# Performance work log

Hardware: AMD Instinct MI355X
Metric: run time of the kernel (lower is better)

## Reference

```python
import jax, jax.numpy as jnp
import numpy as np

B, H, W, C = 3072, 64, 64, 3  # kernel_size=64 forces H=W=64; reshape forces B % 3 == 0


def setup_inputs() -> dict:
    key = jax.random.key(0)
    k0, k1, k2, k3, k4 = jax.random.split(key, 5)
    inputs = jax.random.normal(k0, (B, H, W, C), dtype=jnp.float32)
    # Conv2D(filters=3, kernel_size=64) params, HWIO layout
    w1 = jax.random.normal(k1, (64, 64, 3, 3), dtype=jnp.float32) * 0.02
    b1 = jax.random.normal(k2, (3,), dtype=jnp.float32) * 0.02
    w2 = jax.random.normal(k3, (64, 64, 3, 3), dtype=jnp.float32) * 0.02
    b2 = jax.random.normal(k4, (3,), dtype=jnp.float32) * 0.02
    return {"inputs": inputs, "w1": w1, "b1": b1, "w2": w2, "b2": b2}


def _hilbert_axis1(x):
    # FFT-based Hilbert transform along axis=1 (analytic-signal filter), N even
    N = x.shape[1]
    h = np.zeros(N, dtype=np.float32)
    h[0] = h[N // 2] = 1.0
    h[1:N // 2] = 2.0
    hf = jnp.asarray(h)[None, :, None, None]
    Xf = jnp.fft.fft(x, axis=1)
    return jnp.imag(jnp.fft.ifft(Xf * hf, axis=1)).astype(x.dtype)


def reference(inputs, w1, b1, w2, b2):
    maps_x = inputs[..., :3]                                  # [B,64,64,3]
    b_, h_, w_, c_ = maps_x.shape
    # kernel covers the whole 64x64 image -> 1x1 conv output == full contraction
    v1 = jnp.einsum('bhwc,hwcf->bf', maps_x, w1) + b1          # [B,3]
    v2 = jnp.einsum('bhwc,hwcf->bf', maps_x, w2) + b2          # [B,3]
    V = jnp.stack([v1, v2], axis=-1)                           # [B,3,2]
    V = V / (1e-6 + jnp.sum(jnp.abs(V), axis=1, keepdims=True))
    mx_t = maps_x.reshape(b_, h_ * w_, c_).transpose(0, 2, 1)  # [B,3,HW]
    # Gram matrix and closed-form 2x2 inverse (math of tf.linalg.inv on [B,2,2])
    G = jnp.einsum('bci,bcj->bij', V, V)                       # [B,2,2]
    a = G[:, 0, 0]; bb = G[:, 0, 1]; c = G[:, 1, 0]; d = G[:, 1, 1]
    det = a * d - bb * c
    Ginv = jnp.stack([jnp.stack([d, -bb], -1),
                      jnp.stack([-c, a], -1)], 1) / det[:, None, None]  # [B,2,2]
    Vt_x = jnp.einsum('bck,bcn->bkn', V, mx_t)                 # [B,2,HW]
    rec_t = jnp.einsum('bck,bkn->bcn', V, Ginv @ Vt_x)         # [B,3,HW]
    # lstsq(V, rec_t) via normal equations (tf fast lstsq): z = Ginv V^T rec_t
    z = Ginv @ jnp.einsum('bck,bcn->bkn', V, rec_t)            # [B,2,HW]
    rec = z.transpose(0, 2, 1).reshape(-1, h_, w_, c_)         # [2B/3,64,64,3]
    rec_h = _hilbert_axis1(rec)
    return jnp.concatenate([rec, rec_h], axis=-1)              # [2B/3,64,64,6]
```

## Files before the change

kernel.cpp:

```cpp
#include <hip/hip_runtime.h>
#include <math.h>

#define B_TOT 3072
#define PIX   12288

__global__ __launch_bounds__(256) void compute_M_kernel(
    const float* __restrict__ x, const float* __restrict__ w1,
    const float* __restrict__ b1, const float* __restrict__ w2,
    const float* __restrict__ b2, float* __restrict__ Mout) {
  const int b = blockIdx.x;
  const float4* xb4 = (const float4*)(x + (size_t)b * PIX);
  const float4* w14 = (const float4*)w1;
  const float4* w24 = (const float4*)w2;
  float s[6] = {0, 0, 0, 0, 0, 0};
  for (int i4 = threadIdx.x; i4 < PIX / 4; i4 += 256) {
    float4 xv = xb4[i4];
    float4 a0 = w14[i4 * 3 + 0], a1 = w14[i4 * 3 + 1], a2 = w14[i4 * 3 + 2];
    float4 c0 = w24[i4 * 3 + 0], c1 = w24[i4 * 3 + 1], c2 = w24[i4 * 3 + 2];
    s[0] += xv.x * a0.x + xv.y * a0.w + xv.z * a1.z + xv.w * a2.y;
    s[1] += xv.x * a0.y + xv.y * a1.x + xv.z * a1.w + xv.w * a2.z;
    s[2] += xv.x * a0.z + xv.y * a1.y + xv.z * a2.x + xv.w * a2.w;
    s[3] += xv.x * c0.x + xv.y * c0.w + xv.z * c1.z + xv.w * c2.y;
    s[4] += xv.x * c0.y + xv.y * c1.x + xv.z * c1.w + xv.w * c2.z;
    s[5] += xv.x * c0.z + xv.y * c1.y + xv.z * c2.x + xv.w * c2.w;
  }
  double sd[6];
  #pragma unroll
  for (int j = 0; j < 6; ++j) {
    sd[j] = (double)s[j];
    #pragma unroll
    for (int off = 32; off > 0; off >>= 1)
      sd[j] += __shfl_down(sd[j], off, 64);
  }
  __shared__ double wred[4][6];
  const int wave = threadIdx.x >> 6, lane = threadIdx.x & 63;
  if (lane == 0) {
    #pragma unroll
    for (int j = 0; j < 6; ++j) wred[wave][j] = sd[j];
  }
  __syncthreads();
  if (threadIdx.x == 0) {
    double v[3][2];
    for (int c = 0; c < 3; ++c) {
      v[c][0] = wred[0][c] + wred[1][c] + wred[2][c] + wred[3][c] + (double)b1[c];
      v[c][1] = wred[0][3 + c] + wred[1][3 + c] + wred[2][3 + c] + wred[3][3 + c] + (double)b2[c];
    }
    for (int k = 0; k < 2; ++k) {
      double l1 = 1e-6 + fabs(v[0][k]) + fabs(v[1][k]) + fabs(v[2][k]);
      for (int c = 0; c < 3; ++c) v[c][k] /= l1;
    }
    double G00 = 0, G01 = 0, G11 = 0;
    for (int c = 0; c < 3; ++c) {
      G00 += v[c][0] * v[c][0];
      G01 += v[c][0] * v[c][1];
      G11 += v[c][1] * v[c][1];
    }
    double det = G00 * G11 - G01 * G01;
    double i00 = G11 / det, i01 = -G01 / det, i11 = G00 / det;
    float* Mo = Mout + (size_t)b * 6;
    for (int c = 0; c < 3; ++c) {
      Mo[0 * 3 + c] = (float)(i00 * v[c][0] + i01 * v[c][1]);
      Mo[1 * 3 + c] = (float)(i01 * v[c][0] + i11 * v[c][1]);
    }
  }
}

__global__ __launch_bounds__(192) void z_hilbert_kernel(
    const float* __restrict__ x, const float* __restrict__ M,
    float* __restrict__ out) {
  const int b2 = blockIdx.x;
  __shared__ float rec[PIX];
  __shared__ float Ms[12];
  const size_t zbase = (size_t)b2 * PIX;
  const int b_lo = (int)(zbase >> 13);
  if (threadIdx.x < 12) {
    int bb = b_lo + (int)(threadIdx.x / 6);
    float mv = 0.f;
    if (bb < B_TOT) mv = M[(size_t)bb * 6 + (threadIdx.x % 6)];
    Ms[threadIdx.x] = mv;
  }
  __syncthreads();
  float* outb = out + (size_t)b2 * 24576;

  for (int j = threadIdx.x; j < PIX / 2; j += 192) {
    int ml = j << 1;
    size_t m = zbase + (size_t)ml;
    int b = (int)(m >> 13);
    int n = (int)((m & 8191) >> 1);
    int wb = (b - b_lo) * 6;
    const float* xp = x + (size_t)b * PIX + n * 3;
    float x0 = xp[0], x1 = xp[1], x2 = xp[2];
    float r0 = Ms[wb + 0] * x0 + Ms[wb + 1] * x1 + Ms[wb + 2] * x2;
    float r1 = Ms[wb + 3] * x0 + Ms[wb + 4] * x1 + Ms[wb + 5] * x2;
    float2 rr; rr.x = r0; rr.y = r1;
    ((float2*)rec)[j] = rr;
  }
  __syncthreads();

  {
    const int col = threadIdx.x;
    const int w = col / 3, c = col % 3;
    float gc[16];
    #pragma unroll
    for (int jj = 0; jj < 16; ++jj) {
      float ang = 3.14159265358979323846f * (float)(2 * jj + 1) / 64.0f;
      gc[jj] = 0.03125f * cosf(ang) / sinf(ang);
    }
    float v[64];
    #pragma unroll
    for (int h = 0; h < 64; ++h) v[h] = rec[h * 192 + col];
    float* oc = outb + w * 6 + c;
    #pragma unroll
    for (int h = 0; h < 64; ++h) {
      float acc = 0.f;
      #pragma unroll
      for (int jj = 0; jj < 16; ++jj) {
        int d = 2 * jj + 1;
        acc += gc[jj] * (v[(h - d) & 63] - v[(h + d) & 63]);
      }
      oc[h * 384 + 0] = v[h];
      oc[h * 384 + 3] = acc;
    }
  }
}

extern "C" void kernel_launch(void* const* d_in, const int* in_sizes, int n_in,
                              void* d_out, int out_size, void* d_ws, size_t ws_size,
                              hipStream_t stream) {
  const float* x  = (const float*)d_in[0];
  const float* w1 = (const float*)d_in[1];
  const float* b1 = (const float*)d_in[2];
  const float* w2 = (const float*)d_in[3];
  const float* b2 = (const float*)d_in[4];
  float* out = (float*)d_out;
  float* M = (float*)d_ws;

  compute_M_kernel<<<B_TOT, 256, 0, stream>>>(x, w1, b1, w2, b2, M);
  z_hilbert_kernel<<<2048, 192, 0, stream>>>(x, M, out);
}
```

Measured before the change: 397.2 us.

## Vectorize loads and stores, float shuffle reductions, and nontemporal output writes

In the first kernel the contraction loop is unrolled and the warp reduction uses float shuffles instead of double. The second kernel now runs 256 threads: the rec build reads the input as float4 and writes float4 to shared memory, and the Hilbert stage uses 48 lanes per wave. Those lanes exchange neighbour values with shuffles so each thread writes a contiguous float2 to the output with nontemporal stores. The aim is to cut the number of memory transactions and the cost of the double-precision shuffles, at the price of a quarter of the lanes idling during the Hilbert stage and slightly less precise partial sums.

New measurement: 373.9 us. 5.9% less time.

```diff
diff --git a/kernel.cpp b/kernel.cpp
--- a/kernel.cpp
+++ b/kernel.cpp
@@ -3,6 +3,8 @@
 
 #define B_TOT 3072
 #define PIX   12288
+
+typedef float v2f __attribute__((ext_vector_type(2)));
 
 __global__ __launch_bounds__(256) void compute_M_kernel(
     const float* __restrict__ x, const float* __restrict__ w1,
@@ -13,6 +15,7 @@
   const float4* w14 = (const float4*)w1;
   const float4* w24 = (const float4*)w2;
   float s[6] = {0, 0, 0, 0, 0, 0};
+  #pragma unroll 4
   for (int i4 = threadIdx.x; i4 < PIX / 4; i4 += 256) {
     float4 xv = xb4[i4];
     float4 a0 = w14[i4 * 3 + 0], a1 = w14[i4 * 3 + 1], a2 = w14[i4 * 3 + 2];
@@ -24,26 +27,26 @@
     s[4] += xv.x * c0.y + xv.y * c1.x + xv.z * c1.w + xv.w * c2.z;
     s[5] += xv.x * c0.z + xv.y * c1.y + xv.z * c2.x + xv.w * c2.w;
   }
-  double sd[6];
   #pragma unroll
   for (int j = 0; j < 6; ++j) {
-    sd[j] = (double)s[j];
     #pragma unroll
     for (int off = 32; off > 0; off >>= 1)
-      sd[j] += __shfl_down(sd[j], off, 64);
+      s[j] += __shfl_down(s[j], off, 64);
   }
-  __shared__ double wred[4][6];
+  __shared__ float wred[4][6];
   const int wave = threadIdx.x >> 6, lane = threadIdx.x & 63;
   if (lane == 0) {
     #pragma unroll
-    for (int j = 0; j < 6; ++j) wred[wave][j] = sd[j];
+    for (int j = 0; j < 6; ++j) wred[wave][j] = s[j];
   }
   __syncthreads();
   if (threadIdx.x == 0) {
     double v[3][2];
     for (int c = 0; c < 3; ++c) {
-      v[c][0] = wred[0][c] + wred[1][c] + wred[2][c] + wred[3][c] + (double)b1[c];
-      v[c][1] = wred[0][3 + c] + wred[1][3 + c] + wred[2][3 + c] + wred[3][3 + c] + (double)b2[c];
+      v[c][0] = (double)wred[0][c] + (double)wred[1][c] + (double)wred[2][c] +
+                (double)wred[3][c] + (double)b1[c];
+      v[c][1] = (double)wred[0][3 + c] + (double)wred[1][3 + c] +
+                (double)wred[2][3 + c] + (double)wred[3][3 + c] + (double)b2[c];
     }
     for (int k = 0; k < 2; ++k) {
       double l1 = 1e-6 + fabs(v[0][k]) + fabs(v[1][k]) + fabs(v[2][k]);
@@ -65,11 +68,11 @@
   }
 }
 
-__global__ __launch_bounds__(192) void z_hilbert_kernel(
+__global__ __launch_bounds__(256) void z_hilbert_kernel(
     const float* __restrict__ x, const float* __restrict__ M,
     float* __restrict__ out) {
   const int b2 = blockIdx.x;
-  __shared__ float rec[PIX];
+  __shared__ __align__(16) float rec[PIX];
   __shared__ float Ms[12];
   const size_t zbase = (size_t)b2 * PIX;
   const int b_lo = (int)(zbase >> 13);
@@ -82,24 +85,36 @@
   __syncthreads();
   float* outb = out + (size_t)b2 * 24576;
 
-  for (int j = threadIdx.x; j < PIX / 2; j += 192) {
-    int ml = j << 1;
+  for (int g = threadIdx.x; g < PIX / 8; g += 256) {
+    int ml = g << 3;
     size_t m = zbase + (size_t)ml;
     int b = (int)(m >> 13);
-    int n = (int)((m & 8191) >> 1);
+    int n0 = (int)((m & 8191) >> 1);
     int wb = (b - b_lo) * 6;
-    const float* xp = x + (size_t)b * PIX + n * 3;
-    float x0 = xp[0], x1 = xp[1], x2 = xp[2];
-    float r0 = Ms[wb + 0] * x0 + Ms[wb + 1] * x1 + Ms[wb + 2] * x2;
-    float r1 = Ms[wb + 3] * x0 + Ms[wb + 4] * x1 + Ms[wb + 5] * x2;
-    float2 rr; rr.x = r0; rr.y = r1;
-    ((float2*)rec)[j] = rr;
+    float m00 = Ms[wb + 0], m01 = Ms[wb + 1], m02 = Ms[wb + 2];
+    float m10 = Ms[wb + 3], m11 = Ms[wb + 4], m12 = Ms[wb + 5];
+    const float4* xp = (const float4*)(x + (size_t)b * PIX + (size_t)n0 * 3);
+    float4 p0 = xp[0], p1 = xp[1], p2 = xp[2];
+    float4 o0, o1;
+    o0.x = m00 * p0.x + m01 * p0.y + m02 * p0.z;
+    o0.y = m10 * p0.x + m11 * p0.y + m12 * p0.z;
+    o0.z = m00 * p0.w + m01 * p1.x + m02 * p1.y;
+    o0.w = m10 * p0.w + m11 * p1.x + m12 * p1.y;
+    o1.x = m00 * p1.z + m01 * p1.w + m02 * p2.x;
+    o1.y = m10 * p1.z + m11 * p1.w + m12 * p2.x;
+    o1.z = m00 * p2.y + m01 * p2.z + m02 * p2.w;
+    o1.w = m10 * p2.y + m11 * p2.z + m12 * p2.w;
+    float4* rp = (float4*)&rec[ml];
+    rp[0] = o0;
+    rp[1] = o1;
   }
   __syncthreads();
 
-  {
-    const int col = threadIdx.x;
-    const int w = col / 3, c = col % 3;
+  const int wave = threadIdx.x >> 6, lane = threadIdx.x & 63;
+  if (lane < 48) {
+    const int w = wave * 16 + lane / 3;
+    const int c = lane % 3;
+    const int col = w * 3 + c;
     float gc[16];
     #pragma unroll
     for (int jj = 0; jj < 16; ++jj) {
@@ -109,7 +124,7 @@
     float v[64];
     #pragma unroll
     for (int h = 0; h < 64; ++h) v[h] = rec[h * 192 + col];
-    float* oc = outb + w * 6 + c;
+    float* oc = outb + w * 6 + c * 2;
     #pragma unroll
     for (int h = 0; h < 64; ++h) {
       float acc = 0.f;
@@ -118,8 +133,13 @@
         int d = 2 * jj + 1;
         acc += gc[jj] * (v[(h - d) & 63] - v[(h + d) & 63]);
       }
-      oc[h * 384 + 0] = v[h];
-      oc[h * 384 + 3] = acc;
+      float r = v[h];
+      float s1 = __shfl(r, lane + 1, 64);
+      float s2 = __shfl(acc, lane - 1, 64);
+      v2f st;
+      st.x = (c == 0) ? r : ((c == 1) ? s1 : s2);
+      st.y = (c == 0) ? s1 : ((c == 1) ? s2 : acc);
+      __builtin_nontemporal_store(st, (v2f*)(oc + (size_t)h * 384));
     }
   }
 }
@@ -136,5 +156,5 @@
   float* M = (float*)d_ws;
 
   compute_M_kernel<<<B_TOT, 256, 0, stream>>>(x, w1, b1, w2, b2, M);
-  z_hilbert_kernel<<<2048, 192, 0, stream>>>(x, M, out);
+  z_hilbert_kernel<<<2048, 256, 0, stream>>>(x, M, out);
 }
```
